# Performance work log

Measured on AMD Instinct MI355X. Metric: run time of the kernel, lower is better.

## Reference

```python
import jax, jax.numpy as jnp
import numpy as np

NI = 50000      # input nodes
NO = 50000      # output nodes
DEG = 16        # uniform neighborhood size -> E = NO*DEG
E = NO * DEG
FI = 64         # input feature dim
UNITS = 64
D = 3           # coord feature dim


def setup_inputs() -> dict:
    key = jax.random.key(0)
    k1, k2, k3, k4 = jax.random.split(key, 4)
    node_features = jax.random.normal(k1, (NI, FI), dtype=jnp.float32)
    coord_features = jax.random.normal(k2, (E, D), dtype=jnp.float32)
    indices = jax.random.randint(k3, (E,), 0, NI, dtype=jnp.int64)
    # uniform ragged structure: each output node has DEG edges
    row_splits = (jnp.arange(NO + 1, dtype=jnp.int64) * DEG)
    W = jax.random.normal(k4, (FI, UNITS * D), dtype=jnp.float32) * (1.0 / np.sqrt(FI))
    b = jnp.zeros((UNITS * D,), dtype=jnp.float32)
    return {"node_features": node_features, "coord_features": coord_features,
            "indices": indices, "row_splits": row_splits, "W": W, "b": b}


def reference(node_features, coord_features, indices, row_splits, W, b):
    # Dense projection on input nodes: [Ni, units*D]
    h = node_features @ W + b
    # gather_first=False path of ragged_convolution_transpose: gather after dense
    g = h[indices]                       # [E, units*D]
    g = g.reshape(-1, UNITS, D)          # [E, units, D]
    # contract over coord dim: f_eu = sum_d g_eud * coord_ed
    f = jnp.einsum('eud,ed->eu', g, coord_features)  # [E, units]
    # activation is None (identity)
    # ragged segment-sum via row_splits -> segment ids per edge
    num_out = row_splits.shape[0] - 1
    row_lengths = jnp.diff(row_splits)
    seg_ids = jnp.repeat(jnp.arange(num_out), row_lengths,
                         total_repeat_length=f.shape[0])
    out = jax.ops.segment_sum(f, seg_ids, num_segments=num_out)  # [No, units]
    return out
```

## Files before the change

### kernel.cpp

```cpp
#include <hip/hip_runtime.h>


#define NO 50000
#define NI 50000
#define DEG 16
#define FI 64
#define UNITS 64
#define KK 192
#define TN 16
#define NSTEP 6
#define GPAD 200
#define NBLK 1024
#define NTILES (NO / TN)
#define NFELEM (NI * FI)

typedef __attribute__((ext_vector_type(8))) short short8;
typedef __attribute__((ext_vector_type(4))) float float4v;
typedef __attribute__((ext_vector_type(4))) unsigned int uint4v;
typedef __attribute__((ext_vector_type(4))) unsigned short ushort4v;

static __device__ __forceinline__ unsigned int asu(float x){ union{float f;unsigned int u;}c; c.f=x; return c.u; }
static __device__ __forceinline__ float asf(unsigned int x){ union{unsigned int u;float f;}c; c.u=x; return c.f; }
static __device__ __forceinline__ float rdlane_f(float v, int l){
    return asf((unsigned int)__builtin_amdgcn_readlane((int)asu(v), l));
}
static __device__ __forceinline__ unsigned short f2bf_rne(float x){
    const unsigned int v = asu(x);
    return (unsigned short)((v + 0x7FFFu + ((v >> 16) & 1u)) >> 16);
}

__global__ __launch_bounds__(256)
void rct3_cvt(const float* __restrict__ nf, unsigned short* __restrict__ nf16)
{
    const int i = blockIdx.x * 256 + threadIdx.x;
    const float4v v = ((const float4v*)nf)[i];
    ushort4v o;
    o[0] = f2bf_rne(v[0]); o[1] = f2bf_rne(v[1]);
    o[2] = f2bf_rne(v[2]); o[3] = f2bf_rne(v[3]);
    ((ushort4v*)nf16)[i] = o;
}

template<bool BF16>
__global__ __launch_bounds__(256, 4)
void rct3(const float* __restrict__ nf, const unsigned short* __restrict__ nf16,
          const float* __restrict__ coord, const int* __restrict__ idx,
          const float* __restrict__ W, const float* __restrict__ b,
          float* __restrict__ out)
{
    __shared__ __align__(16) unsigned short Snf[4][64][64];
    __shared__ __align__(16) unsigned short Ghi[TN][GPAD];
    __shared__ __align__(16) float Cs[TN][4];

    const int tid  = threadIdx.x;
    const int w    = tid >> 6;
    const int lane = tid & 63;
    const int m16  = lane & 15;
    const int quad = lane >> 4;

    const int u = 16 * w + m16;
    short8 Bf[NSTEP];
    #pragma unroll
    for (int s = 0; s < NSTEP; ++s) {
        #pragma unroll
        for (int j = 0; j < 8; ++j) {
            const int k = s * 32 + quad * 8 + j;
            const int i = k / 3, d = k - 3 * i;
            Bf[s][j] = (short)f2bf_rne(W[i * KK + 3 * u + d]);
        }
    }
    const float b0 = b[3*u+0], b1 = b[3*u+1], b2 = b[3*u+2];

    int t = blockIdx.x;
    int   vid;
    float cv0, cv1, cv2;
    {
        const int e = (t * TN + 4 * w) * DEG + lane;
        vid = __builtin_nontemporal_load(&idx[e]);
        cv0 = __builtin_nontemporal_load(&coord[3*e+0]);
        cv1 = __builtin_nontemporal_load(&coord[3*e+1]);
        cv2 = __builtin_nontemporal_load(&coord[3*e+2]);
    }

    for (; t < NTILES; t += NBLK) {
        const int node0 = t * TN;

        const int t2 = t + NBLK;
        int   vidN = 0;
        float cv0N = 0.f, cv1N = 0.f, cv2N = 0.f;
        if (t2 < NTILES) {
            const int e2 = (t2 * TN + 4 * w) * DEG + lane;
            vidN = __builtin_nontemporal_load(&idx[e2]);
            cv0N = __builtin_nontemporal_load(&coord[3*e2+0]);
            cv1N = __builtin_nontemporal_load(&coord[3*e2+1]);
            cv2N = __builtin_nontemporal_load(&coord[3*e2+2]);
        }

        __syncthreads();

        {
            float s0 = cv0, s1 = cv1, s2 = cv2;
            #pragma unroll
            for (int m = 1; m <= 8; m <<= 1) {
                s0 += __shfl_xor(s0, m, 64);
                s1 += __shfl_xor(s1, m, 64);
                s2 += __shfl_xor(s2, m, 64);
            }
            if ((lane & 15) == 0) {
                float4v cc = {s0, s1, s2, 0.f};
                *(float4v*)(&Cs[4*w + (lane >> 4)][0]) = cc;
            }
        }

        if constexpr (BF16) {
            uint4v rowreg[8];
            #pragma unroll
            for (int i = 0; i < 8; ++i) {
                const int src = 8 * i + (lane >> 3);
                const int id  = __shfl(vid, src, 64);
                rowreg[i] = *(const uint4v*)((const char*)nf16 +
                              (unsigned long long)id * (FI * 2) + (lane & 7) * 16);
            }
            #pragma unroll
            for (int i = 0; i < 8; ++i) {
                *(uint4v*)((char*)&Snf[w][0][0] + i * 1024 + lane * 16) = rowreg[i];
            }
        }

        #pragma unroll
        for (int r = 0; r < 4; ++r) {
            const int n = 4 * w + r;
            float a0 = 0.f, a1 = 0.f, a2 = 0.f;
            #pragma unroll
            for (int j = 0; j < DEG; ++j) {
                const int l  = 16 * r + j;
                const float c0 = rdlane_f(cv0, l);
                const float c1 = rdlane_f(cv1, l);
                const float c2 = rdlane_f(cv2, l);
                float v;
                if constexpr (BF16) {
                    v = asf(((unsigned int)Snf[w][l][lane]) << 16);
                } else {
                    const int id = __builtin_amdgcn_readlane(vid, l);
                    v = nf[id * FI + lane];
                }
                a0 += v * c0; a1 += v * c1; a2 += v * c2;
            }
            Ghi[n][3*lane+0] = f2bf_rne(a0);
            Ghi[n][3*lane+1] = f2bf_rne(a1);
            Ghi[n][3*lane+2] = f2bf_rne(a2);
        }
        __syncthreads();

        float4v acc = {0.f, 0.f, 0.f, 0.f};
        #pragma unroll
        for (int s = 0; s < NSTEP; ++s) {
            const short8 Ahi = *(const short8*)(&Ghi[m16][s*32 + quad*8]);
            acc = __builtin_amdgcn_mfma_f32_16x16x32_bf16(Ahi, Bf[s], acc, 0, 0, 0);
        }

        #pragma unroll
        for (int reg = 0; reg < 4; ++reg) {
            const int row = quad * 4 + reg;
            const float4v c = *(const float4v*)(&Cs[row][0]);
            out[(node0 + row) * UNITS + u] =
                acc[reg] + c[0]*b0 + c[1]*b1 + c[2]*b2;
        }

        vid = vidN; cv0 = cv0N; cv1 = cv1N; cv2 = cv2N;
    }
}

extern "C" void kernel_launch(void* const* d_in, const int* in_sizes, int n_in,
                              void* d_out, int out_size, void* d_ws, size_t ws_size,
                              hipStream_t stream) {
    const float* nf    = (const float*)d_in[0];
    const float* coord = (const float*)d_in[1];
    const int*   idx   = (const int*)d_in[2];
    const float* W     = (const float*)d_in[4];
    const float* b     = (const float*)d_in[5];
    float* out = (float*)d_out;

    if (ws_size >= (size_t)NFELEM * sizeof(unsigned short)) {
        unsigned short* nf16 = (unsigned short*)d_ws;
        rct3_cvt<<<dim3(NFELEM / 4 / 256), dim3(256), 0, stream>>>(nf, nf16);
        rct3<true><<<dim3(NBLK), dim3(256), 0, stream>>>(
            nf, nf16, coord, idx, W, b, out);
    } else {
        rct3<false><<<dim3(NBLK), dim3(256), 0, stream>>>(
            nf, nullptr, coord, idx, W, b, out);
    }
}
```

Baseline: 107.9 us.

## Software-pipeline bf16 neighbor row gathers one tile ahead with two-deep index prefetch

Issues the gather of bf16 neighbor feature rows for the next tile at the start of each iteration and holds them in registers. They are written to shared memory only after the current tile's compute and stores are done. Index and coord prefetch becomes two tiles deep so the gather addresses are ready a tile early. The aim is to hide the latency of the random row gathers behind the current tile's FMA and MFMA work, in exchange for more registers per thread and possible occupancy loss. Snf is rewritten per wave after the MFMA phase. Only the same wave reads that Snf slice, so no extra barrier should be needed.

Result: no change. 108.8 us (+0.8%).

```diff
diff --git a/kernel.cpp b/kernel.cpp
--- a/kernel.cpp
+++ b/kernel.cpp
@@ -80,19 +80,53 @@
         cv1 = __builtin_nontemporal_load(&coord[3*e+1]);
         cv2 = __builtin_nontemporal_load(&coord[3*e+2]);
     }
+    if constexpr (BF16) {
+        uint4v rr[8];
+        #pragma unroll
+        for (int i = 0; i < 8; ++i) {
+            const int src = 8 * i + (lane >> 3);
+            const int id  = __shfl(vid, src, 64);
+            rr[i] = *(const uint4v*)((const char*)nf16 +
+                      (unsigned long long)id * (FI * 2) + (lane & 7) * 16);
+        }
+        #pragma unroll
+        for (int i = 0; i < 8; ++i)
+            *(uint4v*)((char*)&Snf[w][0][0] + i * 1024 + lane * 16) = rr[i];
+    }
+    int   vidN = 0;
+    float cv0N = 0.f, cv1N = 0.f, cv2N = 0.f;
+    if (t + NBLK < NTILES) {
+        const int e2 = ((t + NBLK) * TN + 4 * w) * DEG + lane;
+        vidN = __builtin_nontemporal_load(&idx[e2]);
+        cv0N = __builtin_nontemporal_load(&coord[3*e2+0]);
+        cv1N = __builtin_nontemporal_load(&coord[3*e2+1]);
+        cv2N = __builtin_nontemporal_load(&coord[3*e2+2]);
+    }
 
     for (; t < NTILES; t += NBLK) {
         const int node0 = t * TN;
-
-        const int t2 = t + NBLK;
-        int   vidN = 0;
-        float cv0N = 0.f, cv1N = 0.f, cv2N = 0.f;
-        if (t2 < NTILES) {
-            const int e2 = (t2 * TN + 4 * w) * DEG + lane;
-            vidN = __builtin_nontemporal_load(&idx[e2]);
-            cv0N = __builtin_nontemporal_load(&coord[3*e2+0]);
-            cv1N = __builtin_nontemporal_load(&coord[3*e2+1]);
-            cv2N = __builtin_nontemporal_load(&coord[3*e2+2]);
+        const int tn    = t + NBLK;
+
+        uint4v rowreg[8];
+        if constexpr (BF16) {
+            if (tn < NTILES) {
+                #pragma unroll
+                for (int i = 0; i < 8; ++i) {
+                    const int src = 8 * i + (lane >> 3);
+                    const int id  = __shfl(vidN, src, 64);
+                    rowreg[i] = *(const uint4v*)((const char*)nf16 +
+                                  (unsigned long long)id * (FI * 2) + (lane & 7) * 16);
+                }
+            }
+        }
+        int   vid2 = 0;
+        float cv02 = 0.f, cv12 = 0.f, cv22 = 0.f;
+        if (tn + NBLK < NTILES) {
+            const int e3 = ((tn + NBLK) * TN + 4 * w) * DEG + lane;
+            vid2 = __builtin_nontemporal_load(&idx[e3]);
+            cv02 = __builtin_nontemporal_load(&coord[3*e3+0]);
+            cv12 = __builtin_nontemporal_load(&coord[3*e3+1]);
+            cv22 = __builtin_nontemporal_load(&coord[3*e3+2]);
         }
 
         __syncthreads();
@@ -108,21 +142,6 @@
             if ((lane & 15) == 0) {
                 float4v cc = {s0, s1, s2, 0.f};
                 *(float4v*)(&Cs[4*w + (lane >> 4)][0]) = cc;
-            }
-        }
-
-        if constexpr (BF16) {
-            uint4v rowreg[8];
-            #pragma unroll
-            for (int i = 0; i < 8; ++i) {
-                const int src = 8 * i + (lane >> 3);
-                const int id  = __shfl(vid, src, 64);
-                rowreg[i] = *(const uint4v*)((const char*)nf16 +
-                              (unsigned long long)id * (FI * 2) + (lane & 7) * 16);
-            }
-            #pragma unroll
-            for (int i = 0; i < 8; ++i) {
-                *(uint4v*)((char*)&Snf[w][0][0] + i * 1024 + lane * 16) = rowreg[i];
             }
         }
 
@@ -166,7 +185,16 @@
                 acc[reg] + c[0]*b0 + c[1]*b1 + c[2]*b2;
         }
 
+        if constexpr (BF16) {
+            if (tn < NTILES) {
+                #pragma unroll
+                for (int i = 0; i < 8; ++i)
+                    *(uint4v*)((char*)&Snf[w][0][0] + i * 1024 + lane * 16) = rowreg[i];
+            }
+        }
+
         vid = vidN; cv0 = cv0N; cv1 = cv1N; cv2 = cv2N;
+        vidN = vid2; cv0N = cv02; cv1N = cv12; cv2N = cv22;
     }
 }
 
```
